# Kernel optimization log

Measured on AMD Instinct MI355X. Metric: run time of the kernel, lower is better.

Reference implementation:

```python
import jax, jax.numpy as jnp
import numpy as np

WS = 7          # window_size
SHIFT = 3       # shift_size
HEADS = 3
DIM = 96
HID = 384       # mlp_ratio * dim
EPS = 1e-5


def _rel_pos_index(ws):
    coords = np.stack(np.meshgrid(np.arange(ws), np.arange(ws), indexing='ij')).reshape(2, -1)
    rel = (coords[:, :, None] - coords[:, None, :]).transpose(1, 2, 0)
    rel[:, :, 0] += ws - 1
    rel[:, :, 1] += ws - 1
    rel[:, :, 0] *= 2 * ws - 1
    return jnp.asarray(rel.sum(-1))  # (ws*ws, ws*ws) int

REL_IDX = _rel_pos_index(WS)


def _shift_mask(H, W):
    # standard Swin SW-MSA mask: (nW, N, N), 0 / -100
    img = np.zeros((H, W), dtype=np.int32)
    cnt = 0
    for h in (slice(0, -WS), slice(-WS, -SHIFT), slice(-SHIFT, None)):
        for w in (slice(0, -WS), slice(-WS, -SHIFT), slice(-SHIFT, None)):
            img[h, w] = cnt
            cnt += 1
    win = img.reshape(H // WS, WS, W // WS, WS).transpose(0, 2, 1, 3).reshape(-1, WS * WS)
    diff = win[:, None, :] - win[:, :, None]
    return jnp.asarray(np.where(diff != 0, -100.0, 0.0).astype(np.float32))


def _ln(x, g, b):
    m = x.mean(-1, keepdims=True)
    v = ((x - m) ** 2).mean(-1, keepdims=True)
    return (x - m) * jax.lax.rsqrt(v + EPS) * g + b


def setup_inputs() -> dict:
    key = jax.random.key(0)
    ks = jax.random.split(key, 12)
    B, H, W, C = 16, 112, 112, DIM
    s = 0.02
    return {
        'x': jax.random.normal(ks[0], (B, H * W, C), jnp.float32),
        'mask': _shift_mask(H, W),
        'norm1_g': jnp.ones((C,), jnp.float32),
        'norm1_b': jnp.zeros((C,), jnp.float32),
        'qkv_w': jax.random.normal(ks[1], (3 * C, C), jnp.float32) * s,
        'qkv_b': jnp.zeros((3 * C,), jnp.float32),
        'rel_bias_table': jax.random.normal(ks[2], ((2 * WS - 1) ** 2, HEADS), jnp.float32) * s,
        'proj_w': jax.random.normal(ks[3], (C, C), jnp.float32) * s,
        'proj_b': jnp.zeros((C,), jnp.float32),
        'norm2_g': jnp.ones((C,), jnp.float32),
        'norm2_b': jnp.zeros((C,), jnp.float32),
        'fc1_w': jax.random.normal(ks[4], (HID, C), jnp.float32) * s,
        'fc1_b': jnp.zeros((HID,), jnp.float32),
        'fc2_w': jax.random.normal(ks[5], (C, HID), jnp.float32) * s,
        'fc2_b': jnp.zeros((C,), jnp.float32),
        'H': 112,
        'W': 112,
    }


def reference(x, mask, norm1_g, norm1_b, qkv_w, qkv_b, rel_bias_table, proj_w,
              proj_b, norm2_g, norm2_b, fc1_w, fc1_b, fc2_w, fc2_b, H, W):
    B, L, C = x.shape
    N = WS * WS
    hd = C // HEADS
    scale = hd ** -0.5
    nh, nw = H // WS, W // WS

    shortcut = x
    h = _ln(x, norm1_g, norm1_b).reshape(B, H, W, C)
    # cyclic shift
    h = jnp.roll(h, (-SHIFT, -SHIFT), axis=(1, 2))
    # window partition -> (B*nW, N, C)
    xw = h.reshape(B, nh, WS, nw, WS, C).transpose(0, 1, 3, 2, 4, 5).reshape(-1, N, C)
    B_ = xw.shape[0]

    qkv = (xw @ qkv_w.T + qkv_b).reshape(B_, N, 3, HEADS, hd).transpose(2, 0, 3, 1, 4)
    q, k, v = qkv[0], qkv[1], qkv[2]          # (B_, heads, N, hd)
    attn = jnp.einsum('bhnd,bhmd->bhnm', q * scale, k)

    bias = rel_bias_table[REL_IDX.reshape(-1)].reshape(N, N, HEADS).transpose(2, 0, 1)
    attn = attn + bias[None]

    nW = mask.shape[0]
    attn = attn.reshape(B_ // nW, nW, HEADS, N, N) + mask[None, :, None]
    attn = jax.nn.softmax(attn.reshape(B_, HEADS, N, N), axis=-1)

    out = jnp.einsum('bhnm,bhmd->bhnd', attn, v).transpose(0, 2, 1, 3).reshape(B_, N, C)
    out = out @ proj_w.T + proj_b

    # window reverse + reverse shift
    out = out.reshape(B, nh, nw, WS, WS, C).transpose(0, 1, 3, 2, 4, 5).reshape(B, H, W, C)
    out = jnp.roll(out, (SHIFT, SHIFT), axis=(1, 2)).reshape(B, L, C)

    x = shortcut + out
    y = _ln(x, norm2_g, norm2_b)
    y = jax.nn.gelu(y @ fc1_w.T + fc1_b, approximate=False)
    y = y @ fc2_w.T + fc2_b
    return x + y
```

## Files before the change

kernel.cpp:

```cpp
#include <hip/hip_runtime.h>
#include <hip/hip_bf16.h>
#include <math.h>


typedef __attribute__((ext_vector_type(8))) short bfrag8;
typedef __attribute__((ext_vector_type(4))) float f32x4;
typedef __attribute__((ext_vector_type(2))) unsigned int u32x2;

#define LOG2E 1.4426950408889634f

__device__ __forceinline__ float bf2f(unsigned short u){
  union { unsigned int i; float f; } c; c.i = ((unsigned int)u) << 16; return c.f;
}
__device__ __forceinline__ unsigned short f2bf(float f){
  __hip_bfloat16 h = __float2bfloat16(f);
  union { __hip_bfloat16 h; unsigned short u; } c; c.h = h; return c.u;
}
__device__ __forceinline__ u32x2 pack4(float a0, float a1, float a2, float a3){
  u32x2 r;
  r.x = (unsigned int)f2bf(a0) | ((unsigned int)f2bf(a1) << 16);
  r.y = (unsigned int)f2bf(a2) | ((unsigned int)f2bf(a3) << 16);
  return r;
}
__device__ __forceinline__ float gelu_f(float x){
  const float c1 = -2.302208198f, c2 = -0.1029432397f;
  float x2 = x * x;
  float t  = __builtin_fmaf(x2, c2, c1);
  float u  = exp2f(x * t);
  return x * __builtin_amdgcn_rcpf(1.f + u);
}

__device__ __forceinline__ int swz32(int r, int c){
  return r * 32 + (c ^ (((r ^ (r >> 2)) & 3) << 3));
}
__device__ __forceinline__ int swz64(int r, int c){
  return r * 64 + (c ^ (((r ^ (r >> 3)) & 7) << 3));
}
__device__ __forceinline__ int fswz(int r, int c){
  return r * 96 + (c ^ ((r & 7) << 2));
}

__device__ __forceinline__ int win_to_img(int r){
  int win = r / 49, n = r - win * 49;
  int b  = win >> 8, wi = win & 255;
  int wh = wi >> 4,  ww = wi & 15;
  int i  = n / 7,    j  = n - i * 7;
  int hs = wh * 7 + i + 3; if (hs >= 112) hs -= 112;
  int ws = ww * 7 + j + 3; if (ws >= 112) ws -= 112;
  return b * 12544 + hs * 112 + ws;
}

__global__ __launch_bounds__(256) void cvt_all_kernel(
    const float* __restrict__ s1, unsigned short* __restrict__ d1,
    const float* __restrict__ s2, unsigned short* __restrict__ d2,
    const float* __restrict__ s3, unsigned short* __restrict__ d3,
    const float* __restrict__ s4, unsigned short* __restrict__ d4,
    const float* __restrict__ bq, float* __restrict__ bqs)
{
  const float QS = 0.17677669529663687f * 1.4426950408889634f;
  int i = blockIdx.x * 256 + threadIdx.x;
  if      (i < 36864)  d1[i]          = f2bf(s1[i]);
  else if (i < 73728)  d2[i - 36864]  = f2bf(s2[i - 36864]);
  else if (i < 101376){
    int j = i - 73728;
    float v = s3[j];
    if (j < 9216) v *= QS;
    d3[j] = f2bf(v);
  }
  else if (i < 110592) d4[i - 101376] = f2bf(s4[i - 101376]);
  else if (i < 110880){
    int j = i - 110592;
    float v = bq[j];
    if (j < 96) v *= QS;
    bqs[j] = v;
  }
}

__global__ __launch_bounds__(256) void cb_kernel(
    const float* __restrict__ relt, const float* __restrict__ mask,
    float* __restrict__ cbt)
{
  int idx = blockIdx.x * 256 + threadIdx.x;
  int ch = idx >> 12;
  int cls = ch / 3, h = ch - cls * 3;
  int w = (cls == 0) ? 0 : (cls == 1) ? 15 : (cls == 2) ? 240 : 255;
  int rem = idx & 4095;
  int mt = rem >> 10, nt = (rem >> 8) & 3, qd = (rem >> 6) & 3;
  int ln = (rem >> 2) & 15, r = rem & 3;
  int m = mt * 16 + qd * 4 + r, n = nt * 16 + ln;
  float v;
  if (m < 49 && n < 49){
    int i1 = m / 7, j1 = m - i1 * 7;
    int i2 = n / 7, j2 = n - i2 * 7;
    int ridx = (i1 - i2 + 6) * 13 + (j1 - j2 + 6);
    v = (relt[ridx * 3 + h] + mask[w * 2401 + m * 49 + n]) * LOG2E;
  } else if (n >= 49) v = -10000.0f;
  else v = 0.0f;
  cbt[idx] = v;
}

__global__ __launch_bounds__(256, 4) void fused_win_kernel(
    const float* __restrict__ x,
    const float* __restrict__ g1, const float* __restrict__ b1n,
    const unsigned short* __restrict__ wqkv, const float* __restrict__ bqs,
    const float* __restrict__ cbt,
    const unsigned short* __restrict__ wproj, const float* __restrict__ bproj,
    unsigned short* __restrict__ x2)
{
  __shared__ unsigned short L[18944];

  int win = blockIdx.x, tid = threadIdx.x;

  {
    int r = tid >> 2, part = tid & 3;
    if (r < 49){
      int gr = win_to_img(win * 49 + r);
      const float* rowp = x + (size_t)gr * 96 + part * 24;
      float v[24]; float s = 0.f, q = 0.f;
      #pragma unroll
      for (int c = 0; c < 24; c++){ v[c] = rowp[c]; s += v[c]; q += v[c] * v[c]; }
      s += __shfl_xor(s, 1); q += __shfl_xor(q, 1);
      s += __shfl_xor(s, 2); q += __shfl_xor(q, 2);
      float mean = s * (1.f / 96.f);
      float rs = rsqrtf(q * (1.f / 96.f) - mean * mean + 1e-5f);
      unsigned short ov[24];
      #pragma unroll
      for (int c = 0; c < 24; c++){
        int cc = part * 24 + c;
        ov[c] = f2bf((v[c] - mean) * rs * g1[cc] + b1n[cc]);
      }
      #pragma unroll
      for (int t = 0; t < 3; t++)
        *reinterpret_cast<bfrag8*>(&L[r * 104 + part * 24 + t * 8]) =
            *reinterpret_cast<const bfrag8*>(&ov[t * 8]);
    } else {
      bfrag8 z = {0, 0, 0, 0, 0, 0, 0, 0};
      #pragma unroll
      for (int t = 0; t < 3; t++)
        *reinterpret_cast<bfrag8*>(&L[r * 104 + part * 24 + t * 8]) = z;
    }
  }
  __syncthreads();

  int wave = tid >> 6, lane = tid & 63;
  int ln = lane & 15, qd = lane >> 4;

  bfrag8 af[4][3];
  #pragma unroll
  for (int mt = 0; mt < 4; mt++)
    #pragma unroll
    for (int k3 = 0; k3 < 3; k3++)
      af[mt][k3] = *reinterpret_cast<const bfrag8*>(
          &L[(mt * 16 + ln) * 104 + k3 * 32 + qd * 8]);
  __syncthreads();

  {
    int nct = (wave < 2) ? 5 : 4;
    for (int i = 0; i < nct; i++){
      int nt = wave + i * 4;
      int col0 = nt * 16;
      const unsigned short* wp = wqkv + (size_t)(col0 + ln) * 96 + qd * 8;
      bfrag8 B0 = *reinterpret_cast<const bfrag8*>(wp);
      bfrag8 B1 = *reinterpret_cast<const bfrag8*>(wp + 32);
      bfrag8 B2 = *reinterpret_cast<const bfrag8*>(wp + 64);
      if (nt < 12){
        f32x4 bs4 = *reinterpret_cast<const f32x4*>(bqs + col0 + qd * 4);
        int c0 = (nt < 6) ? col0 : (col0 - 96);
        int base = 6656 + (c0 >> 5) * 4096 + ((nt < 6) ? 0 : 2048);
        int d0 = (c0 & 31) + qd * 4;
        #pragma unroll
        for (int mt = 0; mt < 4; mt++){
          f32x4 acc = bs4;
          acc = __builtin_amdgcn_mfma_f32_16x16x32_bf16(B0, af[mt][0], acc, 0, 0, 0);
          acc = __builtin_amdgcn_mfma_f32_16x16x32_bf16(B1, af[mt][1], acc, 0, 0, 0);
          acc = __builtin_amdgcn_mfma_f32_16x16x32_bf16(B2, af[mt][2], acc, 0, 0, 0);
          int m = mt * 16 + ln;
          *reinterpret_cast<u32x2*>(&L[base + swz32(m, d0)]) =
              pack4(acc[0], acc[1], acc[2], acc[3]);
        }
      } else {
        int cc = col0 + ln - 192; int hh = cc >> 5, d = cc & 31;
        float bs = bqs[col0 + ln];
        #pragma unroll
        for (int mt = 0; mt < 4; mt++){
          f32x4 acc = {bs, bs, bs, bs};
          acc = __builtin_amdgcn_mfma_f32_16x16x32_bf16(af[mt][0], B0, acc, 0, 0, 0);
          acc = __builtin_amdgcn_mfma_f32_16x16x32_bf16(af[mt][1], B1, acc, 0, 0, 0);
          acc = __builtin_amdgcn_mfma_f32_16x16x32_bf16(af[mt][2], B2, acc, 0, 0, 0);
          int m0 = mt * 16 + qd * 4;
          *reinterpret_cast<u32x2*>(&L[hh * 2048 + swz64(d, m0)]) =
              pack4(acc[0], acc[1], acc[2], acc[3]);
        }
      }
    }
  }
  __syncthreads();

  int h = wave;
  if (wave < 3){
    bfrag8 qf[4];
    #pragma unroll
    for (int mt = 0; mt < 4; mt++)
      qf[mt] = *reinterpret_cast<const bfrag8*>(
          &L[6656 + h * 4096 + swz32(mt * 16 + ln, qd * 8)]);
    int wi = win & 255;
    int cls = (((wi >> 4) == 15) ? 2 : 0) | (((wi & 15) == 15) ? 1 : 0);
    const float* cbh = cbt + ((size_t)cls * 3 + h) * 4096;
    f32x4 sf[4][4];
    #pragma unroll
    for (int nt = 0; nt < 4; nt++){
      bfrag8 kf = *reinterpret_cast<const bfrag8*>(
          &L[6656 + h * 4096 + 2048 + swz32(nt * 16 + ln, qd * 8)]);
      #pragma unroll
      for (int mt = 0; mt < 4; mt++){
        f32x4 cv = *reinterpret_cast<const f32x4*>(
            cbh + mt * 1024 + nt * 256 + qd * 64 + ln * 4);
        sf[mt][nt] = __builtin_amdgcn_mfma_f32_16x16x32_bf16(qf[mt], kf, cv, 0, 0, 0);
      }
    }
    #pragma unroll
    for (int mt = 0; mt < 4; mt++){
      float sm[4];
      #pragma unroll
      for (int r = 0; r < 4; r++){
        float e0 = exp2f(sf[mt][0][r]);
        float e1 = exp2f(sf[mt][1][r]);
        float e2 = exp2f(sf[mt][2][r]);
        float e3 = exp2f(sf[mt][3][r]);
        sf[mt][0][r] = e0; sf[mt][1][r] = e1; sf[mt][2][r] = e2; sf[mt][3][r] = e3;
        sm[r] = e0 + e1 + e2 + e3;
      }
      #pragma unroll
      for (int r = 0; r < 4; r++)
        #pragma unroll
        for (int off = 1; off < 16; off <<= 1)
          sm[r] += __shfl_xor(sm[r], off);
      #pragma unroll
      for (int r = 0; r < 4; r++){
        float inv = __builtin_amdgcn_rcpf(sm[r]);
        int m = mt * 16 + qd * 4 + r;
        #pragma unroll
        for (int nt = 0; nt < 4; nt++)
          L[6656 + h * 4096 + swz64(m, nt * 16 + ln)] = f2bf(sf[mt][nt][r] * inv);
      }
    }

    f32x4 of[4][2];
    #pragma unroll
    for (int mt = 0; mt < 4; mt++)
      #pragma unroll
      for (int dt = 0; dt < 2; dt++) of[mt][dt] = (f32x4){0.f, 0.f, 0.f, 0.f};
    #pragma unroll
    for (int k2 = 0; k2 < 2; k2++){
      bfrag8 vf[2];
      #pragma unroll
      for (int dt = 0; dt < 2; dt++)
        vf[dt] = *reinterpret_cast<const bfrag8*>(
            &L[h * 2048 + swz64(dt * 16 + ln, k2 * 32 + qd * 8)]);
      #pragma unroll
      for (int mt = 0; mt < 4; mt++){
        bfrag8 pf = *reinterpret_cast<const bfrag8*>(
            &L[6656 + h * 4096 + swz64(mt * 16 + ln, k2 * 32 + qd * 8)]);
        #pragma unroll
        for (int dt = 0; dt < 2; dt++)
          of[mt][dt] = __builtin_amdgcn_mfma_f32_16x16x32_bf16(vf[dt], pf, of[mt][dt], 0, 0, 0);
      }
    }
    #pragma unroll
    for (int mt = 0; mt < 4; mt++)
      #pragma unroll
      for (int dt = 0; dt < 2; dt++){
        int m = mt * 16 + ln, d0 = dt * 16 + qd * 4;
        *reinterpret_cast<u32x2*>(&L[h * 2048 + swz32(m, d0)]) =
            pack4(of[mt][dt][0], of[mt][dt][1], of[mt][dt][2], of[mt][dt][3]);
      }
  }
  __syncthreads();

  {
    int rh = wave >> 1, nh = wave & 1;
    bfrag8 ap[2][3];
    #pragma unroll
    for (int mt2 = 0; mt2 < 2; mt2++)
      #pragma unroll
      for (int k3 = 0; k3 < 3; k3++)
        ap[mt2][k3] = *reinterpret_cast<const bfrag8*>(
            &L[k3 * 2048 + swz32(rh * 32 + mt2 * 16 + ln, qd * 8)]);
    float* Xf = reinterpret_cast<float*>(&L[6656]);
    #pragma unroll
    for (int nt3 = 0; nt3 < 3; nt3++){
      int colb = (nh * 3 + nt3) * 16;
      const unsigned short* wp = wproj + (size_t)(colb + ln) * 96 + qd * 8;
      bfrag8 B0 = *reinterpret_cast<const bfrag8*>(wp);
      bfrag8 B1 = *reinterpret_cast<const bfrag8*>(wp + 32);
      bfrag8 B2 = *reinterpret_cast<const bfrag8*>(wp + 64);
      f32x4 bv4 = *reinterpret_cast<const f32x4*>(bproj + colb + qd * 4);
      #pragma unroll
      for (int mt2 = 0; mt2 < 2; mt2++){
        f32x4 acc = bv4;
        acc = __builtin_amdgcn_mfma_f32_16x16x32_bf16(B0, ap[mt2][0], acc, 0, 0, 0);
        acc = __builtin_amdgcn_mfma_f32_16x16x32_bf16(B1, ap[mt2][1], acc, 0, 0, 0);
        acc = __builtin_amdgcn_mfma_f32_16x16x32_bf16(B2, ap[mt2][2], acc, 0, 0, 0);
        int m = rh * 32 + mt2 * 16 + ln;
        *reinterpret_cast<f32x4*>(&Xf[fswz(m, colb + qd * 4)]) = acc;
      }
    }
  }
  __syncthreads();

  {
    int r = tid >> 2, part = tid & 3;
    if (r < 49){
      int gi = win_to_img(win * 49 + r);
      const float* Xf = reinterpret_cast<const float*>(&L[6656]);
      const float* rowp = x + (size_t)gi * 96 + part * 24;
      int sxm = (r & 7) << 2;
      unsigned short ov[24];
      #pragma unroll
      for (int t6 = 0; t6 < 6; t6++){
        int cc = part * 24 + t6 * 4;
        f32x4 pv = *reinterpret_cast<const f32x4*>(&Xf[r * 96 + (cc ^ sxm)]);
        f32x4 rv = *reinterpret_cast<const f32x4*>(&rowp[t6 * 4]);
        #pragma unroll
        for (int j = 0; j < 4; j++)
          ov[t6 * 4 + j] = f2bf(pv[j] + rv[j]);
      }
      unsigned short* dst = x2 + (size_t)gi * 96 + part * 24;
      #pragma unroll
      for (int t3 = 0; t3 < 3; t3++)
        *reinterpret_cast<bfrag8*>(dst + t3 * 8) =
            *reinterpret_cast<const bfrag8*>(&ov[t3 * 8]);
    }
  }
}

__global__ __launch_bounds__(384, 4) void mlp_mfma_kernel(
    const unsigned short* __restrict__ x2,
    const float* __restrict__ g, const float* __restrict__ b,
    const unsigned short* __restrict__ w1, const float* __restrict__ b1,
    const unsigned short* __restrict__ w2, const float* __restrict__ b2,
    float* __restrict__ out)
{
  __shared__ unsigned short S[25088];
  unsigned short* As = S;
  unsigned short* Hs = S;
  int tid = threadIdx.x;
  int row0 = blockIdx.x * 64;

  if (tid < 256){
    int rr = tid >> 2, part = tid & 3;
    const unsigned short* rp = x2 + (size_t)(row0 + rr) * 96 + part * 24;
    float v[24]; float s = 0.f, q = 0.f;
    #pragma unroll
    for (int t = 0; t < 3; t++){
      bfrag8 w = *reinterpret_cast<const bfrag8*>(rp + t * 8);
      #pragma unroll
      for (int j = 0; j < 8; j++){
        float f = bf2f((unsigned short)w[j]);
        v[t * 8 + j] = f; s += f; q += f * f;
      }
    }
    s += __shfl_xor(s, 1); q += __shfl_xor(q, 1);
    s += __shfl_xor(s, 2); q += __shfl_xor(q, 2);
    float mean = s * (1.f / 96.f);
    float rs = rsqrtf(q * (1.f / 96.f) - mean * mean + 1e-5f);
    unsigned short ov[24];
    #pragma unroll
    for (int c = 0; c < 24; c++){
      int cc = part * 24 + c;
      ov[c] = f2bf((v[c] - mean) * rs * g[cc] + b[cc]);
    }
    #pragma unroll
    for (int t = 0; t < 3; t++)
      *reinterpret_cast<bfrag8*>(&As[rr * 104 + part * 24 + t * 8]) =
          *reinterpret_cast<const bfrag8*>(&ov[t * 8]);
  }
  __syncthreads();

  int wave = tid / 64, lane = tid & 63;
  int ln = lane & 15, qd = lane >> 4;

  bfrag8 af[4][3];
  #pragma unroll
  for (int mt = 0; mt < 4; mt++)
    #pragma unroll
    for (int k3 = 0; k3 < 3; k3++)
      af[mt][k3] = *reinterpret_cast<const bfrag8*>(
          &As[(mt * 16 + ln) * 104 + k3 * 32 + qd * 8]);
  __syncthreads();

  for (int i = 0; i < 4; i++){
    int ntl = wave + i * 6;
    int col0 = ntl * 16;
    const unsigned short* wp = w1 + (size_t)(col0 + ln) * 96 + qd * 8;
    bfrag8 B0 = *reinterpret_cast<const bfrag8*>(wp);
    bfrag8 B1 = *reinterpret_cast<const bfrag8*>(wp + 32);
    bfrag8 B2 = *reinterpret_cast<const bfrag8*>(wp + 64);
    f32x4 bs4 = *reinterpret_cast<const f32x4*>(b1 + col0 + qd * 4);
    #pragma unroll
    for (int mt = 0; mt < 4; mt++){
      f32x4 a = bs4;
      a = __builtin_amdgcn_mfma_f32_16x16x32_bf16(B0, af[mt][0], a, 0, 0, 0);
      a = __builtin_amdgcn_mfma_f32_16x16x32_bf16(B1, af[mt][1], a, 0, 0, 0);
      a = __builtin_amdgcn_mfma_f32_16x16x32_bf16(B2, af[mt][2], a, 0, 0, 0);
      int m = mt * 16 + ln;
      *reinterpret_cast<u32x2*>(&Hs[m * 392 + col0 + qd * 4]) =
          pack4(gelu_f(a[0]), gelu_f(a[1]), gelu_f(a[2]), gelu_f(a[3]));
    }
  }
  __syncthreads();

  int col0 = wave * 16;
  f32x4 bs4 = *reinterpret_cast<const f32x4*>(b2 + col0 + qd * 4);
  f32x4 acc[4];
  #pragma unroll
  for (int mt = 0; mt < 4; mt++) acc[mt] = bs4;
  for (int k2 = 0; k2 < 12; k2++){
    bfrag8 B = *reinterpret_cast<const bfrag8*>(
        w2 + (size_t)(col0 + ln) * 384 + k2 * 32 + qd * 8);
    #pragma unroll
    for (int mt = 0; mt < 4; mt++){
      bfrag8 p = *reinterpret_cast<const bfrag8*>(
          &Hs[(mt * 16 + ln) * 392 + k2 * 32 + qd * 8]);
      acc[mt] = __builtin_amdgcn_mfma_f32_16x16x32_bf16(B, p, acc[mt], 0, 0, 0);
    }
  }
  {
    #pragma unroll
    for (int mt = 0; mt < 4; mt++){
      int grow = row0 + mt * 16 + ln;
      u32x2 rv = *reinterpret_cast<const u32x2*>(
          x2 + (size_t)grow * 96 + col0 + qd * 4);
      f32x4 o;
      o[0] = acc[mt][0] + bf2f((unsigned short)(rv.x & 0xffff));
      o[1] = acc[mt][1] + bf2f((unsigned short)(rv.x >> 16));
      o[2] = acc[mt][2] + bf2f((unsigned short)(rv.y & 0xffff));
      o[3] = acc[mt][3] + bf2f((unsigned short)(rv.y >> 16));
      *reinterpret_cast<f32x4*>(out + (size_t)grow * 96 + col0 + qd * 4) = o;
    }
  }
}

extern "C" void kernel_launch(void* const* d_in, const int* in_sizes, int n_in,
                              void* d_out, int out_size, void* d_ws, size_t ws_size,
                              hipStream_t stream)
{
  const float* x      = (const float*)d_in[0];
  const float* mask   = (const float*)d_in[1];
  const float* n1g    = (const float*)d_in[2];
  const float* n1b    = (const float*)d_in[3];
  const float* qkv_w  = (const float*)d_in[4];
  const float* qkv_b  = (const float*)d_in[5];
  const float* relt   = (const float*)d_in[6];
  const float* proj_w = (const float*)d_in[7];
  const float* proj_b = (const float*)d_in[8];
  const float* n2g    = (const float*)d_in[9];
  const float* n2b    = (const float*)d_in[10];
  const float* fc1_w  = (const float*)d_in[11];
  const float* fc1_b  = (const float*)d_in[12];
  const float* fc2_w  = (const float*)d_in[13];
  const float* fc2_b  = (const float*)d_in[14];
  float* outp = (float*)d_out;
  (void)in_sizes; (void)n_in; (void)out_size; (void)ws_size; (void)mask;

  const size_t M = 200704;
  char* ws = (char*)d_ws;
  unsigned short* x2     = (unsigned short*)ws;
  size_t o = M * 96 * 2;
  unsigned short* w1bf   = (unsigned short*)(ws + o); o += 384 * 96 * 2;
  unsigned short* w2bf   = (unsigned short*)(ws + o); o += 96 * 384 * 2;
  unsigned short* wqkvbf = (unsigned short*)(ws + o); o += 288 * 96 * 2;
  unsigned short* wprojbf= (unsigned short*)(ws + o); o += 96 * 96 * 2;
  float*          bqs    = (float*)(ws + o);          o += 288 * 4 + 64;
  float*          cbuf   = (float*)(ws + o); o += (size_t)4 * 3 * 4096 * 4;

  cvt_all_kernel<<<434, 256, 0, stream>>>(
      fc1_w, w1bf, fc2_w, w2bf, qkv_w, wqkvbf, proj_w, wprojbf, qkv_b, bqs);
  cb_kernel<<<192, 256, 0, stream>>>(relt, mask, cbuf);
  fused_win_kernel<<<4096, 256, 0, stream>>>(
      x, n1g, n1b, wqkvbf, bqs, cbuf, wprojbf, proj_b, x2);
  mlp_mfma_kernel<<<3136, 384, 0, stream>>>(
      x2, n2g, n2b, w1bf, fc1_b, w2bf, fc2_b, outp);
}
```

Measured before the change: 299.4 us.

## Overlap second half of fc1 with first half of fc2 in MLP kernel

The MLP kernel now computes the first 192 hidden columns, syncs, and then interleaves computing the remaining hidden columns with fc2 accumulation over the first 192 columns. After a second barrier it finishes fc2 over the remaining columns. The aim is to overlap fc1 GELU/MFMA work with fc2 MFMAs and LDS reads, hiding latency within waves. It adds an extra barrier and unrolled loops, which increases register pressure.

```diff
diff --git a/kernel.cpp b/kernel.cpp
--- a/kernel.cpp
+++ b/kernel.cpp
@@ -389,7 +389,8 @@
           &As[(mt * 16 + ln) * 104 + k3 * 32 + qd * 8]);
   __syncthreads();
 
-  for (int i = 0; i < 4; i++){
+  #pragma unroll
+  for (int i = 0; i < 2; i++){
     int ntl = wave + i * 6;
     int col0 = ntl * 16;
     const unsigned short* wp = w1 + (size_t)(col0 + ln) * 96 + qd * 8;
@@ -410,14 +411,51 @@
   }
   __syncthreads();
 
-  int col0 = wave * 16;
-  f32x4 bs4 = *reinterpret_cast<const f32x4*>(b2 + col0 + qd * 4);
+  int oc0 = wave * 16;
+  f32x4 obs4 = *reinterpret_cast<const f32x4*>(b2 + oc0 + qd * 4);
   f32x4 acc[4];
   #pragma unroll
-  for (int mt = 0; mt < 4; mt++) acc[mt] = bs4;
-  for (int k2 = 0; k2 < 12; k2++){
+  for (int mt = 0; mt < 4; mt++) acc[mt] = obs4;
+
+  #pragma unroll
+  for (int i = 0; i < 2; i++){
+    {
+      int ntl = wave + 12 + i * 6;
+      int col0 = ntl * 16;
+      const unsigned short* wp = w1 + (size_t)(col0 + ln) * 96 + qd * 8;
+      bfrag8 B0 = *reinterpret_cast<const bfrag8*>(wp);
+      bfrag8 B1 = *reinterpret_cast<const bfrag8*>(wp + 32);
+      bfrag8 B2 = *reinterpret_cast<const bfrag8*>(wp + 64);
+      f32x4 bs4 = *reinterpret_cast<const f32x4*>(b1 + col0 + qd * 4);
+      #pragma unroll
+      for (int mt = 0; mt < 4; mt++){
+        f32x4 a = bs4;
+        a = __builtin_amdgcn_mfma_f32_16x16x32_bf16(B0, af[mt][0], a, 0, 0, 0);
+        a = __builtin_amdgcn_mfma_f32_16x16x32_bf16(B1, af[mt][1], a, 0, 0, 0);
+        a = __builtin_amdgcn_mfma_f32_16x16x32_bf16(B2, af[mt][2], a, 0, 0, 0);
+        int m = mt * 16 + ln;
+        *reinterpret_cast<u32x2*>(&Hs[m * 392 + col0 + qd * 4]) =
+            pack4(gelu_f(a[0]), gelu_f(a[1]), gelu_f(a[2]), gelu_f(a[3]));
+      }
+    }
+    #pragma unroll
+    for (int k2 = i * 3; k2 < i * 3 + 3; k2++){
+      bfrag8 B = *reinterpret_cast<const bfrag8*>(
+          w2 + (size_t)(oc0 + ln) * 384 + k2 * 32 + qd * 8);
+      #pragma unroll
+      for (int mt = 0; mt < 4; mt++){
+        bfrag8 p = *reinterpret_cast<const bfrag8*>(
+            &Hs[(mt * 16 + ln) * 392 + k2 * 32 + qd * 8]);
+        acc[mt] = __builtin_amdgcn_mfma_f32_16x16x32_bf16(B, p, acc[mt], 0, 0, 0);
+      }
+    }
+  }
+  __syncthreads();
+
+  #pragma unroll
+  for (int k2 = 6; k2 < 12; k2++){
     bfrag8 B = *reinterpret_cast<const bfrag8*>(
-        w2 + (size_t)(col0 + ln) * 384 + k2 * 32 + qd * 8);
+        w2 + (size_t)(oc0 + ln) * 384 + k2 * 32 + qd * 8);
     #pragma unroll
     for (int mt = 0; mt < 4; mt++){
       bfrag8 p = *reinterpret_cast<const bfrag8*>(
@@ -425,18 +463,19 @@
       acc[mt] = __builtin_amdgcn_mfma_f32_16x16x32_bf16(B, p, acc[mt], 0, 0, 0);
     }
   }
+
   {
     #pragma unroll
     for (int mt = 0; mt < 4; mt++){
       int grow = row0 + mt * 16 + ln;
       u32x2 rv = *reinterpret_cast<const u32x2*>(
-          x2 + (size_t)grow * 96 + col0 + qd * 4);
+          x2 + (size_t)grow * 96 + oc0 + qd * 4);
       f32x4 o;
       o[0] = acc[mt][0] + bf2f((unsigned short)(rv.x & 0xffff));
       o[1] = acc[mt][1] + bf2f((unsigned short)(rv.x >> 16));
       o[2] = acc[mt][2] + bf2f((unsigned short)(rv.y & 0xffff));
       o[3] = acc[mt][3] + bf2f((unsigned short)(rv.y >> 16));
-      *reinterpret_cast<f32x4*>(out + (size_t)grow * 96 + col0 + qd * 4) = o;
+      *reinterpret_cast<f32x4*>(out + (size_t)grow * 96 + oc0 + qd * 4) = o;
     }
   }
 }
```

Result: no change. 298.8 us (-0.2%).
